# Optimization experiments

Measured on AMD Instinct MI355X. Metric: run time of the kernel, lower is better.

Reference implementation:

```python
import jax, jax.numpy as jnp
import numpy as np

N, E = 50000, 800000
F_IN, H = 64, 64
DEPTH, LAYERS = 3, 2


def setup_inputs() -> dict:
    key = jax.random.key(0)
    ks = jax.random.split(key, 14)
    z = jax.random.normal(ks[0], (N, F_IN), dtype=jnp.float32)
    edge_index = jax.random.randint(ks[1], (2, E), 0, N, dtype=jnp.int64)
    s = 1.0 / np.sqrt(H)
    u = lambda k, shape: jax.random.uniform(k, shape, jnp.float32, -s, s)
    return dict(
        z=z, edge_index=edge_index,
        # GRU layer 0 (input F_IN), torch gate order r,z,n
        W_ih0=u(ks[2], (3 * H, F_IN)), W_hh0=u(ks[3], (3 * H, H)),
        b_ih0=u(ks[4], (3 * H,)), b_hh0=u(ks[5], (3 * H,)),
        # GRU layer 1 (input H)
        W_ih1=u(ks[6], (3 * H, H)), W_hh1=u(ks[7], (3 * H, H)),
        b_ih1=u(ks[8], (3 * H,)), b_hh1=u(ks[9], (3 * H,)),
        # output head: Tanh -> Linear(H, 1)
        W_out=u(ks[10], (1, H)), b_out=u(ks[11], (1,)),
    )


def _mean_aggr(h, src, dst, n_nodes):
    # scatter-mean of neighbor (src) states into dst nodes
    msg = jax.ops.segment_sum(h[src], dst, num_segments=n_nodes)  # [N, F]
    cnt = jax.ops.segment_sum(jnp.ones((src.shape[0],), h.dtype), dst,
                              num_segments=n_nodes)
    return msg / jnp.maximum(cnt, 1.0)[:, None]


def _gru_cell(x, h, W_ih, W_hh, b_ih, b_hh):
    gi = x @ W_ih.T + b_ih          # [N, 3H]
    gh = h @ W_hh.T + b_hh
    i_r, i_z, i_n = jnp.split(gi, 3, axis=-1)
    h_r, h_z, h_n = jnp.split(gh, 3, axis=-1)
    r = jax.nn.sigmoid(i_r + h_r)
    zt = jax.nn.sigmoid(i_z + h_z)
    n = jnp.tanh(i_n + r * h_n)
    return (1.0 - zt) * n + zt * h


def _run_gru_layer(xs, W_ih, W_hh, b_ih, b_hh):
    # xs: [T, N, F]; returns (outputs [T, N, H], last hidden [N, H])
    h0 = jnp.zeros((xs.shape[1], W_hh.shape[1]), xs.dtype)

    def step(h, x):
        h2 = _gru_cell(x, h, W_ih, W_hh, b_ih, b_hh)
        return h2, h2

    hT, ys = jax.lax.scan(step, h0, xs)
    return ys, hT


def reference(z, edge_index, W_ih0, W_hh0, b_ih0, b_hh0,
              W_ih1, W_hh1, b_ih1, b_hh1, W_out, b_out):
    src, dst = edge_index[0], edge_index[1]
    n_nodes = z.shape[0]
    # Build the tree-depth sequence: original z followed by DEPTH rounds of
    # mean message passing (irregular gather-aggregate-scatter per depth).
    seq = [z]
    h = z
    for _ in range(DEPTH):
        h = _mean_aggr(h, src, dst, n_nodes)
        seq.append(h)
    xs = jnp.stack(seq, axis=0)  # [DEPTH+1, N, F_IN]
    ys, _ = _run_gru_layer(xs, W_ih0, W_hh0, b_ih0, b_hh0)
    _, hT = _run_gru_layer(ys, W_ih1, W_hh1, b_ih1, b_hh1)  # top layer final state
    return jnp.tanh(hT) @ W_out.T + b_out  # [N, 1]
```

## Files before the change

kernel.cpp:

```cpp
#include <hip/hip_runtime.h>
#include <hip/hip_bf16.h>

#define N_NODES 50000
#define N_EDGES 800000

typedef __attribute__((ext_vector_type(8))) short short8;
typedef __attribute__((ext_vector_type(4))) float f32x4;

__device__ __forceinline__ unsigned short f2bf_hi(float f) {
    unsigned u = __float_as_uint(f);
    unsigned r = u + 0x7fffu + ((u >> 16) & 1u);
    return (unsigned short)(r >> 16);
}
__device__ __forceinline__ float bf2f(unsigned short h) {
    return __uint_as_float(((unsigned)h) << 16);
}
__device__ __forceinline__ float u2f(unsigned u) { return __uint_as_float(u); }

__device__ __forceinline__ unsigned pack_bf2(float a, float b) {
    float2 t{a, b};
    __hip_bfloat162 r = __float22bfloat162_rn(t);
    return *reinterpret_cast<unsigned*>(&r);
}

__device__ __forceinline__ float sigm_(float v) {
    return __builtin_amdgcn_rcpf(1.0f + __expf(-v));
}
__device__ __forceinline__ float tanh2_(float a) {
    float e = __expf(-2.0f * a);
    return fmaf(2.0f, __builtin_amdgcn_rcpf(1.0f + e), -1.0f);
}


__global__ __launch_bounds__(256) void count_kernel(const int* __restrict__ ei,
                                                    int* __restrict__ deg) {
    int e = blockIdx.x * 256 + threadIdx.x;
    if (e < N_EDGES) atomicAdd(&deg[ei[N_EDGES + e]], 1);
}

__global__ __launch_bounds__(256) void scan_part(const int* __restrict__ deg,
                                                 int* __restrict__ part) {
    __shared__ int sm[256];
    int b = blockIdx.x, t = threadIdx.x;
    int s = 0;
#pragma unroll
    for (int i = 0; i < 4; ++i) {
        int idx = b * 1024 + i * 256 + t;
        if (idx < N_NODES) s += deg[idx];
    }
    sm[t] = s;
    __syncthreads();
    for (int off = 128; off; off >>= 1) {
        if (t < off) sm[t] += sm[t + off];
        __syncthreads();
    }
    if (t == 0) part[b] = sm[0];
}

__global__ __launch_bounds__(64) void scan_top(const int* __restrict__ part,
                                               int* __restrict__ pref) {
    int lane = threadIdx.x;
    int v = (lane < 49) ? part[lane] : 0;
    for (int off = 1; off < 64; off <<= 1) {
        int u = __shfl_up(v, off);
        if (lane >= off) v += u;
    }
    if (lane == 0) pref[0] = 0;
    if (lane < 49) pref[lane + 1] = v;
}

__global__ __launch_bounds__(1024) void scan_final(const int* __restrict__ deg,
                                                   const int* __restrict__ pref,
                                                   int* __restrict__ rowptr,
                                                   int* __restrict__ cur) {
    __shared__ int sm[1024];
    int b = blockIdx.x, t = threadIdx.x;
    int idx = b * 1024 + t;
    int d = (idx < N_NODES) ? deg[idx] : 0;
    sm[t] = d;
    __syncthreads();
    for (int off = 1; off < 1024; off <<= 1) {
        int u = (t >= off) ? sm[t - off] : 0;
        __syncthreads();
        sm[t] += u;
        __syncthreads();
    }
    int excl = pref[b] + sm[t] - d;
    if (idx < N_NODES) {
        rowptr[idx] = excl;
        cur[idx] = excl;
    } else if (idx == N_NODES) {
        rowptr[idx] = excl;
    }
}

__global__ __launch_bounds__(256) void fill_kernel(const int* __restrict__ ei,
                                                   int* __restrict__ cur,
                                                   int* __restrict__ col) {
    int e = blockIdx.x * 256 + threadIdx.x;
    if (e < N_EDGES) {
        int s = ei[e];
        int d = ei[N_EDGES + e];
        int p = atomicAdd(&cur[d], 1);
        col[p] = s;
    }
}


__global__ __launch_bounds__(256) void gather_kernel(const int* __restrict__ rowptr,
                                                     const int* __restrict__ col,
                                                     const float* __restrict__ src,
                                                     float* __restrict__ dst) {
    int node = (blockIdx.x * 256 + threadIdx.x) >> 6;
    if (node >= N_NODES) return;
    const int lane = threadIdx.x & 63;
    const int g = lane >> 4;
    const int l16 = lane & 15;
    const int beg = rowptr[node], end = rowptr[node + 1];
    const float4* s4 = reinterpret_cast<const float4*>(src);

    float4 a0 = {0.f, 0.f, 0.f, 0.f}, a1 = {0.f, 0.f, 0.f, 0.f};
#pragma unroll 1
    for (int e = beg + 2 * g; e < end; e += 8) {
        int c0 = col[e];
        float4 v0 = s4[c0 * 16 + l16];
        if (e + 1 < end) {
            int c1 = col[e + 1];
            float4 v1 = s4[c1 * 16 + l16];
            a1.x += v1.x; a1.y += v1.y; a1.z += v1.z; a1.w += v1.w;
        }
        a0.x += v0.x; a0.y += v0.y; a0.z += v0.z; a0.w += v0.w;
    }
    a0.x += a1.x; a0.y += a1.y; a0.z += a1.z; a0.w += a1.w;
#pragma unroll
    for (int m = 16; m <= 32; m <<= 1) {
        a0.x += __shfl_xor(a0.x, m);
        a0.y += __shfl_xor(a0.y, m);
        a0.z += __shfl_xor(a0.z, m);
        a0.w += __shfl_xor(a0.w, m);
    }
    if (g == 0) {
        float inv = __builtin_amdgcn_rcpf(fmaxf((float)(end - beg), 1.0f));
        float4 r = {a0.x * inv, a0.y * inv, a0.z * inv, a0.w * inv};
        reinterpret_cast<float4*>(dst)[node * 16 + l16] = r;
    }
}


__global__ __launch_bounds__(256) void wprep_kernel(
    const float* __restrict__ Wih0, const float* __restrict__ Whh0,
    const float* __restrict__ Wih1, const float* __restrict__ Whh1,
    unsigned short* __restrict__ wout) {
    int idx = blockIdx.x * 256 + threadIdx.x;
    if (idx >= 49152) return;
    int e = idx & 7;
    int lane = (idx >> 3) & 63;
    int ks = (idx >> 9) & 1;
    int r = idx >> 10;
    int ct = r % 12;
    int mat = (r / 12) & 1;
    int layer = r / 24;
    const float* W = layer ? (mat ? Whh1 : Wih1) : (mat ? Whh0 : Wih0);
    int j = ct * 16 + (lane & 15);
    int k = ks * 32 + ((lane >> 4) << 3) + e;
    float v = W[j * 64 + k];
    unsigned short hi = f2bf_hi(v);
    unsigned short lo = f2bf_hi(v - bf2f(hi));
    int base = layer * 49152 + mat * 24576 + ct * 2048 + ks * 1024;
    wout[base + lane * 8 + e] = hi;
    wout[base + 512 + lane * 8 + e] = lo;
}


__device__ __forceinline__ f32x4 mfma_bf16(short8 a, short8 b, f32x4 c) {
    return __builtin_amdgcn_mfma_f32_16x16x32_bf16(a, b, c, 0, 0, 0);
}

template <int LAYER>
__device__ __forceinline__ void gru_cell_mfma(
    int ct, int col16, int kgrp, int tid,
    const short8 (&wf)[2][2][2][2],
    float bias_a, float bias_b,
    const unsigned short (*Ahi)[72], const unsigned short (*Alo)[72],
    unsigned short (&Hhi)[2][32][72], unsigned short (&Hlo)[2][32][72],
    float (&G)[32][196], float (&Gn2)[32][68]) {
    f32x4 acc_a[2], acc_b[2];
#pragma unroll
    for (int rt = 0; rt < 2; ++rt) {
        acc_a[rt] = {bias_a, bias_a, bias_a, bias_a};
        acc_b[rt] = {bias_b, bias_b, bias_b, bias_b};
    }
#pragma unroll
    for (int rt = 0; rt < 2; ++rt) {
#pragma unroll
        for (int ks = 0; ks < 2; ++ks) {
            const int row = rt * 16 + col16;
            const int koff = ks * 32 + kgrp;
            short8 a_in_hi = *reinterpret_cast<const short8*>(&Ahi[row][koff]);
            short8 a_in_lo = *reinterpret_cast<const short8*>(&Alo[row][koff]);
            short8 a_h_hi = *reinterpret_cast<const short8*>(&Hhi[LAYER][row][koff]);
            short8 a_h_lo = *reinterpret_cast<const short8*>(&Hlo[LAYER][row][koff]);
            short8 bi0 = wf[LAYER][0][ks][0], bi1 = wf[LAYER][0][ks][1];
            short8 bh0 = wf[LAYER][1][ks][0], bh1 = wf[LAYER][1][ks][1];
            acc_a[rt] = mfma_bf16(a_in_hi, bi0, acc_a[rt]);
            acc_a[rt] = mfma_bf16(a_in_hi, bi1, acc_a[rt]);
            acc_a[rt] = mfma_bf16(a_in_lo, bi0, acc_a[rt]);
            if (ct < 8) {
                acc_a[rt] = mfma_bf16(a_h_hi, bh0, acc_a[rt]);
                acc_a[rt] = mfma_bf16(a_h_hi, bh1, acc_a[rt]);
                acc_a[rt] = mfma_bf16(a_h_lo, bh0, acc_a[rt]);
            } else {
                acc_b[rt] = mfma_bf16(a_h_hi, bh0, acc_b[rt]);
                acc_b[rt] = mfma_bf16(a_h_hi, bh1, acc_b[rt]);
                acc_b[rt] = mfma_bf16(a_h_lo, bh0, acc_b[rt]);
            }
        }
    }
    const int q4 = (kgrp >> 3) * 4;
    const int gcol = ct * 16 + col16;
#pragma unroll
    for (int rt = 0; rt < 2; ++rt) {
#pragma unroll
        for (int v = 0; v < 4; ++v) {
            int grow = rt * 16 + q4 + v;
            G[grow][gcol] = acc_a[rt][v];
            if (ct >= 8) Gn2[grow][gcol - 128] = acc_b[rt][v];
        }
    }
    __syncthreads();
    if (tid < 512) {
#pragma unroll
        for (int h2 = 0; h2 < 2; ++h2) {
            int p = tid + h2 * 512;
            int m = p >> 5, j0 = (p & 31) * 2;
            float gr0 = G[m][j0],       gr1 = G[m][j0 + 1];
            float gz0 = G[m][64 + j0],  gz1 = G[m][64 + j0 + 1];
            float gn0 = G[m][128 + j0], gn1 = G[m][128 + j0 + 1];
            float gm0 = Gn2[m][j0],     gm1 = Gn2[m][j0 + 1];
            unsigned hhi = *reinterpret_cast<const unsigned*>(&Hhi[LAYER][m][j0]);
            unsigned hlo = *reinterpret_cast<const unsigned*>(&Hlo[LAYER][m][j0]);
            float hold0 = u2f(hhi << 16) + u2f(hlo << 16);
            float hold1 = u2f(hhi & 0xffff0000u) + u2f(hlo & 0xffff0000u);
            float r0 = sigm_(gr0), r1 = sigm_(gr1);
            float z0 = sigm_(gz0), z1 = sigm_(gz1);
            float n0 = tanh2_(fmaf(r0, gm0, gn0));
            float n1 = tanh2_(fmaf(r1, gm1, gn1));
            float h0 = fmaf(z0, hold0 - n0, n0);
            float h1 = fmaf(z1, hold1 - n1, n1);
            unsigned phi = pack_bf2(h0, h1);
            float l0 = h0 - u2f(phi << 16);
            float l1 = h1 - u2f(phi & 0xffff0000u);
            unsigned plo = pack_bf2(l0, l1);
            *reinterpret_cast<unsigned*>(&Hhi[LAYER][m][j0]) = phi;
            *reinterpret_cast<unsigned*>(&Hlo[LAYER][m][j0]) = plo;
        }
    }
    __syncthreads();
}

__global__ __launch_bounds__(768) void gru_kernel(
    const float* __restrict__ x0, const float* __restrict__ x1,
    const float* __restrict__ x2, const float* __restrict__ x3,
    const unsigned short* __restrict__ wprep,
    const float* __restrict__ bih0, const float* __restrict__ bhh0,
    const float* __restrict__ bih1, const float* __restrict__ bhh1,
    const float* __restrict__ Wout, const float* __restrict__ bout,
    float* __restrict__ out) {
    __shared__ __align__(16) float G[32][196];
    __shared__ __align__(16) float Gn2[32][68];
    __shared__ __align__(16) unsigned short Hhi[2][32][72];
    __shared__ __align__(16) unsigned short Hlo[2][32][72];
    __shared__ __align__(16) unsigned short Xhi[32][72];
    __shared__ __align__(16) unsigned short Xlo[32][72];

    const int tid = threadIdx.x;
    const int lane = tid & 63;
    const int ct = tid >> 6;
    const int col16 = lane & 15;
    const int kgrp = (lane >> 4) << 3;
    const int nodebase = blockIdx.x * 32;

    short8 wf[2][2][2][2];
    {
        const short8* wp = reinterpret_cast<const short8*>(wprep);
#pragma unroll
        for (int layer = 0; layer < 2; ++layer)
#pragma unroll
            for (int mat = 0; mat < 2; ++mat)
#pragma unroll
                for (int ks = 0; ks < 2; ++ks)
#pragma unroll
                    for (int term = 0; term < 2; ++term)
                        wf[layer][mat][ks][term] =
                            wp[(layer * 49152 + mat * 24576 + ct * 2048 +
                                ks * 1024 + term * 512 + lane * 8) >> 3];
    }
    const int gcol = ct * 16 + col16;
    float bias0_a, bias0_b, bias1_a, bias1_b;
    if (ct < 8) {
        bias0_a = bih0[gcol] + bhh0[gcol]; bias0_b = 0.0f;
        bias1_a = bih1[gcol] + bhh1[gcol]; bias1_b = 0.0f;
    } else {
        bias0_a = bih0[gcol]; bias0_b = bhh0[gcol];
        bias1_a = bih1[gcol]; bias1_b = bhh1[gcol];
    }

    for (int i = tid; i < 2304; i += 768) {
        reinterpret_cast<unsigned*>(&Hhi[0][0][0])[i] = 0;
        reinterpret_cast<unsigned*>(&Hlo[0][0][0])[i] = 0;
    }
    __syncthreads();

#pragma unroll 1
    for (int t = 0; t < 4; ++t) {
        const float* xp = (t == 0) ? x0 : (t == 1) ? x1 : (t == 2) ? x2 : x3;
        if (tid < 512) {
#pragma unroll
            for (int h2 = 0; h2 < 2; ++h2) {
                int p = tid + h2 * 512;
                int m = p >> 5, k0 = (p & 31) * 2;
                int node = nodebase + m;
                if (node >= N_NODES) node = N_NODES - 1;
                float2 v = *reinterpret_cast<const float2*>(xp + (size_t)node * 64 + k0);
                unsigned phi = pack_bf2(v.x, v.y);
                float l0 = v.x - u2f(phi << 16);
                float l1 = v.y - u2f(phi & 0xffff0000u);
                *reinterpret_cast<unsigned*>(&Xhi[m][k0]) = phi;
                *reinterpret_cast<unsigned*>(&Xlo[m][k0]) = pack_bf2(l0, l1);
            }
        }
        __syncthreads();
        gru_cell_mfma<0>(ct, col16, kgrp, tid, wf, bias0_a, bias0_b,
                         Xhi, Xlo, Hhi, Hlo, G, Gn2);
        gru_cell_mfma<1>(ct, col16, kgrp, tid, wf, bias1_a, bias1_b,
                         Hhi[0], Hlo[0], Hhi, Hlo, G, Gn2);
    }

    if (tid < 512) {
        int m = tid >> 4, l16 = tid & 15;
        float acc = 0.0f;
#pragma unroll
        for (int q = 0; q < 4; ++q) {
            int j = l16 * 4 + q;
            float h = bf2f(Hhi[1][m][j]) + bf2f(Hlo[1][m][j]);
            acc = fmaf(tanh2_(h), Wout[j], acc);
        }
        acc += __shfl_down(acc, 8, 16);
        acc += __shfl_down(acc, 4, 16);
        acc += __shfl_down(acc, 2, 16);
        acc += __shfl_down(acc, 1, 16);
        int node = nodebase + m;
        if (l16 == 0 && node < N_NODES) out[node] = acc + bout[0];
    }
}

extern "C" void kernel_launch(void* const* d_in, const int* in_sizes, int n_in,
                              void* d_out, int out_size, void* d_ws, size_t ws_size,
                              hipStream_t stream) {
    const float* z    = (const float*)d_in[0];
    const int*   ei   = (const int*)d_in[1];
    const float* Wih0 = (const float*)d_in[2];
    const float* Whh0 = (const float*)d_in[3];
    const float* bih0 = (const float*)d_in[4];
    const float* bhh0 = (const float*)d_in[5];
    const float* Wih1 = (const float*)d_in[6];
    const float* Whh1 = (const float*)d_in[7];
    const float* bih1 = (const float*)d_in[8];
    const float* bhh1 = (const float*)d_in[9];
    const float* Wout = (const float*)d_in[10];
    const float* bout = (const float*)d_in[11];
    float* out = (float*)d_out;
    float* ws  = (float*)d_ws;

    float* x1 = ws;
    float* x2 = x1 + 3200000;
    float* x3 = x2 + 3200000;
    unsigned short* wprep = (unsigned short*)(x3 + 3200000);
    int* rowptr = (int*)(ws + 9600000 + 49152);
    int* deg    = rowptr + 50004;
    int* cur    = deg + 50000;
    int* col    = cur + 50000;
    int* part   = col + 800000;
    int* pref   = part + 64;

    hipMemsetAsync(deg, 0, 50000 * sizeof(int), stream);

    wprep_kernel<<<192, 256, 0, stream>>>(Wih0, Whh0, Wih1, Whh1, wprep);
    count_kernel<<<(N_EDGES + 255) / 256, 256, 0, stream>>>(ei, deg);
    scan_part<<<49, 256, 0, stream>>>(deg, part);
    scan_top<<<1, 64, 0, stream>>>(part, pref);
    scan_final<<<49, 1024, 0, stream>>>(deg, pref, rowptr, cur);
    fill_kernel<<<(N_EDGES + 255) / 256, 256, 0, stream>>>(ei, cur, col);

    gather_kernel<<<(N_NODES * 64 + 255) / 256, 256, 0, stream>>>(rowptr, col, z, x1);
    gather_kernel<<<(N_NODES * 64 + 255) / 256, 256, 0, stream>>>(rowptr, col, x1, x2);
    gather_kernel<<<(N_NODES * 64 + 255) / 256, 256, 0, stream>>>(rowptr, col, x2, x3);

    gru_kernel<<<(N_NODES + 31) / 32, 768, 0, stream>>>(
        z, x1, x2, x3, wprep, bih0, bhh0, bih1, bhh1, Wout, bout, out);
}
```

Before: 385.3 us.

## Overlap next-step input staging with GRU elementwise and fuse scan kernels

```diff
diff --git a/kernel.cpp b/kernel.cpp
--- a/kernel.cpp
+++ b/kernel.cpp
@@ -57,24 +57,19 @@
     if (t == 0) part[b] = sm[0];
 }
 
-__global__ __launch_bounds__(64) void scan_top(const int* __restrict__ part,
-                                               int* __restrict__ pref) {
-    int lane = threadIdx.x;
-    int v = (lane < 49) ? part[lane] : 0;
-    for (int off = 1; off < 64; off <<= 1) {
-        int u = __shfl_up(v, off);
-        if (lane >= off) v += u;
-    }
-    if (lane == 0) pref[0] = 0;
-    if (lane < 49) pref[lane + 1] = v;
-}
-
 __global__ __launch_bounds__(1024) void scan_final(const int* __restrict__ deg,
-                                                   const int* __restrict__ pref,
+                                                   const int* __restrict__ part,
                                                    int* __restrict__ rowptr,
                                                    int* __restrict__ cur) {
     __shared__ int sm[1024];
+    __shared__ int basep;
     int b = blockIdx.x, t = threadIdx.x;
+    if (t < 64) {
+        int v = (t < b) ? part[t] : 0;
+#pragma unroll
+        for (int off = 1; off < 64; off <<= 1) v += __shfl_xor(v, off);
+        if (t == 0) basep = v;
+    }
     int idx = b * 1024 + t;
     int d = (idx < N_NODES) ? deg[idx] : 0;
     sm[t] = d;
@@ -85,7 +80,7 @@
         sm[t] += u;
         __syncthreads();
     }
-    int excl = pref[b] + sm[t] - d;
+    int excl = basep + sm[t] - d;
     if (idx < N_NODES) {
         rowptr[idx] = excl;
         cur[idx] = excl;
@@ -120,18 +115,31 @@
     const float4* s4 = reinterpret_cast<const float4*>(src);
 
     float4 a0 = {0.f, 0.f, 0.f, 0.f}, a1 = {0.f, 0.f, 0.f, 0.f};
+    float4 a2 = {0.f, 0.f, 0.f, 0.f}, a3 = {0.f, 0.f, 0.f, 0.f};
 #pragma unroll 1
-    for (int e = beg + 2 * g; e < end; e += 8) {
+    for (int e = beg + 4 * g; e < end; e += 16) {
         int c0 = col[e];
         float4 v0 = s4[c0 * 16 + l16];
+        a0.x += v0.x; a0.y += v0.y; a0.z += v0.z; a0.w += v0.w;
         if (e + 1 < end) {
             int c1 = col[e + 1];
             float4 v1 = s4[c1 * 16 + l16];
             a1.x += v1.x; a1.y += v1.y; a1.z += v1.z; a1.w += v1.w;
         }
-        a0.x += v0.x; a0.y += v0.y; a0.z += v0.z; a0.w += v0.w;
+        if (e + 2 < end) {
+            int c2 = col[e + 2];
+            float4 v2 = s4[c2 * 16 + l16];
+            a2.x += v2.x; a2.y += v2.y; a2.z += v2.z; a2.w += v2.w;
+        }
+        if (e + 3 < end) {
+            int c3 = col[e + 3];
+            float4 v3 = s4[c3 * 16 + l16];
+            a3.x += v3.x; a3.y += v3.y; a3.z += v3.z; a3.w += v3.w;
+        }
     }
     a0.x += a1.x; a0.y += a1.y; a0.z += a1.z; a0.w += a1.w;
+    a2.x += a3.x; a2.y += a3.y; a2.z += a3.z; a2.w += a3.w;
+    a0.x += a2.x; a0.y += a2.y; a0.z += a2.z; a0.w += a2.w;
 #pragma unroll
     for (int m = 16; m <= 32; m <<= 1) {
         a0.x += __shfl_xor(a0.x, m);
@@ -177,8 +185,8 @@
 }
 
 template <int LAYER>
-__device__ __forceinline__ void gru_cell_mfma(
-    int ct, int col16, int kgrp, int tid,
+__device__ __forceinline__ void mfma_phase(
+    int ct, int col16, int kgrp,
     const short8 (&wf)[2][2][2][2],
     float bias_a, float bias_b,
     const unsigned short (*Ahi)[72], const unsigned short (*Alo)[72],
@@ -227,35 +235,49 @@
             if (ct >= 8) Gn2[grow][gcol - 128] = acc_b[rt][v];
         }
     }
-    __syncthreads();
-    if (tid < 512) {
-#pragma unroll
-        for (int h2 = 0; h2 < 2; ++h2) {
-            int p = tid + h2 * 512;
-            int m = p >> 5, j0 = (p & 31) * 2;
-            float gr0 = G[m][j0],       gr1 = G[m][j0 + 1];
-            float gz0 = G[m][64 + j0],  gz1 = G[m][64 + j0 + 1];
-            float gn0 = G[m][128 + j0], gn1 = G[m][128 + j0 + 1];
-            float gm0 = Gn2[m][j0],     gm1 = Gn2[m][j0 + 1];
-            unsigned hhi = *reinterpret_cast<const unsigned*>(&Hhi[LAYER][m][j0]);
-            unsigned hlo = *reinterpret_cast<const unsigned*>(&Hlo[LAYER][m][j0]);
-            float hold0 = u2f(hhi << 16) + u2f(hlo << 16);
-            float hold1 = u2f(hhi & 0xffff0000u) + u2f(hlo & 0xffff0000u);
-            float r0 = sigm_(gr0), r1 = sigm_(gr1);
-            float z0 = sigm_(gz0), z1 = sigm_(gz1);
-            float n0 = tanh2_(fmaf(r0, gm0, gn0));
-            float n1 = tanh2_(fmaf(r1, gm1, gn1));
-            float h0 = fmaf(z0, hold0 - n0, n0);
-            float h1 = fmaf(z1, hold1 - n1, n1);
-            unsigned phi = pack_bf2(h0, h1);
-            float l0 = h0 - u2f(phi << 16);
-            float l1 = h1 - u2f(phi & 0xffff0000u);
-            unsigned plo = pack_bf2(l0, l1);
-            *reinterpret_cast<unsigned*>(&Hhi[LAYER][m][j0]) = phi;
-            *reinterpret_cast<unsigned*>(&Hlo[LAYER][m][j0]) = plo;
-        }
-    }
-    __syncthreads();
+}
+
+template <int LAYER>
+__device__ __forceinline__ void ew_pair(
+    int p,
+    unsigned short (&Hhi)[2][32][72], unsigned short (&Hlo)[2][32][72],
+    float (&G)[32][196], float (&Gn2)[32][68]) {
+    int m = p >> 5, j0 = (p & 31) * 2;
+    float2 gr = *reinterpret_cast<const float2*>(&G[m][j0]);
+    float2 gz = *reinterpret_cast<const float2*>(&G[m][64 + j0]);
+    float2 gn = *reinterpret_cast<const float2*>(&G[m][128 + j0]);
+    float2 gm = *reinterpret_cast<const float2*>(&Gn2[m][j0]);
+    unsigned hhi = *reinterpret_cast<const unsigned*>(&Hhi[LAYER][m][j0]);
+    unsigned hlo = *reinterpret_cast<const unsigned*>(&Hlo[LAYER][m][j0]);
+    float hold0 = u2f(hhi << 16) + u2f(hlo << 16);
+    float hold1 = u2f(hhi & 0xffff0000u) + u2f(hlo & 0xffff0000u);
+    float r0 = sigm_(gr.x), r1 = sigm_(gr.y);
+    float z0 = sigm_(gz.x), z1 = sigm_(gz.y);
+    float n0 = tanh2_(fmaf(r0, gm.x, gn.x));
+    float n1 = tanh2_(fmaf(r1, gm.y, gn.y));
+    float h0 = fmaf(z0, hold0 - n0, n0);
+    float h1 = fmaf(z1, hold1 - n1, n1);
+    unsigned phi = pack_bf2(h0, h1);
+    float l0 = h0 - u2f(phi << 16);
+    float l1 = h1 - u2f(phi & 0xffff0000u);
+    unsigned plo = pack_bf2(l0, l1);
+    *reinterpret_cast<unsigned*>(&Hhi[LAYER][m][j0]) = phi;
+    *reinterpret_cast<unsigned*>(&Hlo[LAYER][m][j0]) = plo;
+}
+
+__device__ __forceinline__ void stage_pair(const float* __restrict__ xp, int nodebase,
+                                           int p,
+                                           unsigned short (&Xhi)[32][72],
+                                           unsigned short (&Xlo)[32][72]) {
+    int m = p >> 5, k0 = (p & 31) * 2;
+    int node = nodebase + m;
+    if (node >= N_NODES) node = N_NODES - 1;
+    float2 v = *reinterpret_cast<const float2*>(xp + (size_t)node * 64 + k0);
+    unsigned phi = pack_bf2(v.x, v.y);
+    float l0 = v.x - u2f(phi << 16);
+    float l1 = v.y - u2f(phi & 0xffff0000u);
+    *reinterpret_cast<unsigned*>(&Xhi[m][k0]) = phi;
+    *reinterpret_cast<unsigned*>(&Xlo[m][k0]) = pack_bf2(l0, l1);
 }
 
 __global__ __launch_bounds__(768) void gru_kernel(
@@ -309,31 +331,33 @@
         reinterpret_cast<unsigned*>(&Hhi[0][0][0])[i] = 0;
         reinterpret_cast<unsigned*>(&Hlo[0][0][0])[i] = 0;
     }
+    stage_pair(x0, nodebase, tid, Xhi, Xlo);
+    if (tid < 256) stage_pair(x0, nodebase, tid + 768, Xhi, Xlo);
     __syncthreads();
 
 #pragma unroll 1
     for (int t = 0; t < 4; ++t) {
-        const float* xp = (t == 0) ? x0 : (t == 1) ? x1 : (t == 2) ? x2 : x3;
+        mfma_phase<0>(ct, col16, kgrp, wf, bias0_a, bias0_b,
+                      Xhi, Xlo, Hhi, Hlo, G, Gn2);
+        __syncthreads();
+        ew_pair<0>(tid, Hhi, Hlo, G, Gn2);
+        if (tid < 256) ew_pair<0>(tid + 768, Hhi, Hlo, G, Gn2);
+        __syncthreads();
+        mfma_phase<1>(ct, col16, kgrp, wf, bias1_a, bias1_b,
+                      Hhi[0], Hlo[0], Hhi, Hlo, G, Gn2);
+        __syncthreads();
         if (tid < 512) {
-#pragma unroll
-            for (int h2 = 0; h2 < 2; ++h2) {
-                int p = tid + h2 * 512;
-                int m = p >> 5, k0 = (p & 31) * 2;
-                int node = nodebase + m;
-                if (node >= N_NODES) node = N_NODES - 1;
-                float2 v = *reinterpret_cast<const float2*>(xp + (size_t)node * 64 + k0);
-                unsigned phi = pack_bf2(v.x, v.y);
-                float l0 = v.x - u2f(phi << 16);
-                float l1 = v.y - u2f(phi & 0xffff0000u);
-                *reinterpret_cast<unsigned*>(&Xhi[m][k0]) = phi;
-                *reinterpret_cast<unsigned*>(&Xlo[m][k0]) = pack_bf2(l0, l1);
-            }
-        }
-        __syncthreads();
-        gru_cell_mfma<0>(ct, col16, kgrp, tid, wf, bias0_a, bias0_b,
-                         Xhi, Xlo, Hhi, Hlo, G, Gn2);
-        gru_cell_mfma<1>(ct, col16, kgrp, tid, wf, bias1_a, bias1_b,
-                         Hhi[0], Hlo[0], Hhi, Hlo, G, Gn2);
+            ew_pair<1>(tid, Hhi, Hlo, G, Gn2);
+            ew_pair<1>(tid + 512, Hhi, Hlo, G, Gn2);
+        } else if (t < 3) {
+            const float* xn = (t == 0) ? x1 : (t == 1) ? x2 : x3;
+            int q = tid - 512;
+            stage_pair(xn, nodebase, q, Xhi, Xlo);
+            stage_pair(xn, nodebase, q + 256, Xhi, Xlo);
+            stage_pair(xn, nodebase, q + 512, Xhi, Xlo);
+            stage_pair(xn, nodebase, q + 768, Xhi, Xlo);
+        }
+        __syncthreads();
     }
 
     if (tid < 512) {
@@ -381,15 +405,13 @@
     int* cur    = deg + 50000;
     int* col    = cur + 50000;
     int* part   = col + 800000;
-    int* pref   = part + 64;
 
     hipMemsetAsync(deg, 0, 50000 * sizeof(int), stream);
 
     wprep_kernel<<<192, 256, 0, stream>>>(Wih0, Whh0, Wih1, Whh1, wprep);
     count_kernel<<<(N_EDGES + 255) / 256, 256, 0, stream>>>(ei, deg);
     scan_part<<<49, 256, 0, stream>>>(deg, part);
-    scan_top<<<1, 64, 0, stream>>>(part, pref);
-    scan_final<<<49, 1024, 0, stream>>>(deg, pref, rowptr, cur);
+    scan_final<<<49, 1024, 0, stream>>>(deg, part, rowptr, cur);
     fill_kernel<<<(N_EDGES + 255) / 256, 256, 0, stream>>>(ei, cur, col);
 
     gather_kernel<<<(N_NODES * 64 + 255) / 256, 256, 0, stream>>>(rowptr, col, z, x1);
```

Result: no change. 389.9 us (+1.2%).
